# Kernel tuning notes

Measured on AMD Instinct MI355X. Metric: run time of the kernel, lower is better.

Reference implementation:

```python
import jax, jax.numpy as jnp
import numpy as np

MARGIN = 0.3
HARD_FACTOR = 0.0
NO_POS = 1000000.0
BIG = jnp.finfo(jnp.float32).max


def setup_inputs() -> dict:
    key = jax.random.key(0)
    k1, k2 = jax.random.split(key)
    global_feat = jax.random.normal(k1, (4096, 256), dtype=jnp.float32)
    labels = jax.random.randint(k2, (4096,), 0, 512, dtype=jnp.int64)
    return {"global_feat": global_feat, "labels": labels}


def euclidean_dist(x, y):
    # [m, n] pairwise distances via GEMM trick, clamped before sqrt
    xx = jnp.sum(x * x, axis=1, keepdims=True)          # [m, 1]
    yy = jnp.sum(y * y, axis=1, keepdims=True).T        # [1, n]
    d2 = xx + yy - 2.0 * (x @ y.T)
    return jnp.sqrt(jnp.maximum(d2, 1e-12))


def reference(global_feat, labels):
    feat = global_feat.astype(jnp.float32)
    dist_mat = euclidean_dist(feat, feat)               # [N, N]

    is_pos = labels[None, :] == labels[:, None]         # [N, N]
    is_neg = ~is_pos

    # hardest positive: masked row max; hardest negative: masked row min
    pos_max = jnp.max(jnp.where(is_pos, dist_mat, -BIG), axis=1)
    neg_min = jnp.min(jnp.where(is_neg, dist_mat, BIG), axis=1)
    has_pos = jnp.any(is_pos, axis=1)
    has_neg = jnp.any(is_neg, axis=1)
    dist_ap = jnp.where(has_pos, pos_max, NO_POS)
    dist_an = jnp.where(has_neg, neg_min, 0.0)

    dist_ap = dist_ap * (1.0 + HARD_FACTOR)
    dist_an = dist_an * (1.0 - HARD_FACTOR)

    valid = (dist_ap < NO_POS) & (dist_an > 0)
    n_valid = jnp.sum(valid.astype(jnp.float32))

    # MarginRankingLoss(y=1): mean over valid of relu(margin + dist_ap - dist_an)
    per_elem = jnp.maximum(MARGIN + dist_ap - dist_an, 0.0)
    loss_sum = jnp.sum(jnp.where(valid, per_elem, 0.0))
    loss = jnp.where(n_valid > 0, loss_sum / jnp.maximum(n_valid, 1.0), 0.0)
    return loss
```

## Files before the change

kernel.cpp:

```cpp
#include <hip/hip_runtime.h>
#include <hip/hip_bf16.h>

#define N 4096
#define D 256
#define MARGIN 0.3f
#define NSLOT 33
#define FLT_BIG 3.402823466e+38f

typedef __attribute__((ext_vector_type(8))) short short8;
typedef __attribute__((ext_vector_type(4))) float f32x4;
typedef const __attribute__((address_space(1))) unsigned char g1_t;
typedef __attribute__((address_space(3))) unsigned char l3_t;

__device__ __forceinline__ ushort f2bf(float f) {
    unsigned u = __float_as_uint(f);
    unsigned r = (u + 0x7fffu + ((u >> 16) & 1u)) >> 16;
    return (ushort)r;
}

__global__ __launch_bounds__(256) void prep_kernel(
        const float* __restrict__ feat,
        float* __restrict__ xx,
        ushort* __restrict__ hi,
        float* __restrict__ gacc,
        unsigned* __restrict__ ticket) {
    if (blockIdx.x == 0 && threadIdx.x == 0) {
        gacc[0] = 0.0f; gacc[1] = 0.0f; *ticket = 0u;
    }
    int row  = blockIdx.x * 4 + (threadIdx.x >> 6);
    int lane = threadIdx.x & 63;
    float4 v = *(const float4*)(feat + row * D + lane * 4);
    *(ushort4*)(hi + row * D + lane * 4) =
        make_ushort4(f2bf(v.x), f2bf(v.y), f2bf(v.z), f2bf(v.w));
    float s = v.x * v.x + v.y * v.y + v.z * v.z + v.w * v.w;
    #pragma unroll
    for (int off = 32; off >= 1; off >>= 1) s += __shfl_xor(s, off);
    if (lane == 0) xx[row] = s;
}

__global__ __launch_bounds__(256, 2) void dist_mfma_kernel(
        const ushort* __restrict__ hi,
        const int* __restrict__ labels, const float* __restrict__ xx,
        float* __restrict__ pPart, float* __restrict__ nPart) {
    __shared__ __attribute__((aligned(16))) short sA[2][128 * 64];
    __shared__ __attribute__((aligned(16))) short sB[2][128 * 64];
    __shared__ float rp[4][64], rn[4][64], cp[4][64], cn[4][64];

    int t = blockIdx.x, bi = 0, rem = 32;
    while (t >= rem) { t -= rem; ++bi; --rem; }
    const int bj = bi + t;
    const int rowBase = bi * 128;
    const int colBase = bj * 128;

    const int tid  = threadIdx.x;
    const int lane = tid & 63;
    const int wid  = tid >> 6;
    const int wr   = (wid >> 1) * 64;
    const int wc   = (wid & 1) * 64;
    const int l15  = lane & 15;
    const int kq   = (lane >> 4) * 8;
    const int swz  = (lane & 7) << 3;

    f32x4 acc[4][4] = {};

    auto stage = [&](int b, int kt) {
        #pragma unroll
        for (int i = 0; i < 4; ++i) {
            int c   = i * 256 + tid;
            int row = c >> 3;
            int kc  = ((c ^ row) & 7) * 8;
            __builtin_amdgcn_global_load_lds(
                (g1_t*)(hi + (size_t)(rowBase + row) * D + kt + kc),
                (l3_t*)(&sA[b][c * 8]), 16, 0, 0);
            __builtin_amdgcn_global_load_lds(
                (g1_t*)(hi + (size_t)(colBase + row) * D + kt + kc),
                (l3_t*)(&sB[b][c * 8]), 16, 0, 0);
        }
    };

    stage(0, 0);
    __syncthreads();
    int cur = 0;
    for (int step = 0; step < 4; ++step) {
        if (step < 3) stage(cur ^ 1, (step + 1) * 64);
        #pragma unroll
        for (int h = 0; h < 2; ++h) {
            short8 af[4], bfv[4];
            #pragma unroll
            for (int m = 0; m < 4; ++m) {
                int idx = ((wr + m * 16 + l15) << 6) + h * 32 + kq;
                af[m] = *(const short8*)(&sA[cur][idx ^ swz]);
            }
            #pragma unroll
            for (int n = 0; n < 4; ++n) {
                int idx = ((wc + n * 16 + l15) << 6) + h * 32 + kq;
                bfv[n] = *(const short8*)(&sB[cur][idx ^ swz]);
            }
            #pragma unroll
            for (int m = 0; m < 4; ++m)
                #pragma unroll
                for (int n = 0; n < 4; ++n)
                    acc[m][n] = __builtin_amdgcn_mfma_f32_16x16x32_bf16(
                        af[m], bfv[n], acc[m][n], 0, 0, 0);
        }
        __syncthreads();
        cur ^= 1;
    }

    float xr[4][4]; int lrow[4][4];
    #pragma unroll
    for (int m = 0; m < 4; ++m)
        #pragma unroll
        for (int j = 0; j < 4; ++j) {
            int rg = rowBase + wr + m * 16 + (lane >> 4) * 4 + j;
            xr[m][j] = xx[rg]; lrow[m][j] = labels[rg];
        }
    float xc[4]; int lcol[4];
    #pragma unroll
    for (int n = 0; n < 4; ++n) {
        int cg = colBase + wc + n * 16 + l15;
        xc[n] = xx[cg]; lcol[n] = labels[cg];
    }

    float pm2[4][4], nm2[4][4];
    float cpm[4],   cnm[4];
    #pragma unroll
    for (int m = 0; m < 4; ++m)
        #pragma unroll
        for (int j = 0; j < 4; ++j) { pm2[m][j] = 0.0f; nm2[m][j] = FLT_BIG; }
    #pragma unroll
    for (int n = 0; n < 4; ++n) { cpm[n] = 0.0f; cnm[n] = FLT_BIG; }

    #pragma unroll
    for (int m = 0; m < 4; ++m)
        #pragma unroll
        for (int n = 0; n < 4; ++n)
            #pragma unroll
            for (int j = 0; j < 4; ++j) {
                float d2 = fmaxf(xr[m][j] + xc[n] - 2.0f * acc[m][n][j], 0.0f);
                bool pos = (lrow[m][j] == lcol[n]);
                if (pos) {
                    pm2[m][j] = fmaxf(pm2[m][j], d2);
                    cpm[n]    = fmaxf(cpm[n],    d2);
                } else {
                    nm2[m][j] = fminf(nm2[m][j], d2);
                    cnm[n]    = fminf(cnm[n],    d2);
                }
            }

    #pragma unroll
    for (int m = 0; m < 4; ++m)
        #pragma unroll
        for (int j = 0; j < 4; ++j) {
            #pragma unroll
            for (int off = 1; off <= 8; off <<= 1) {
                pm2[m][j] = fmaxf(pm2[m][j], __shfl_xor(pm2[m][j], off));
                nm2[m][j] = fminf(nm2[m][j], __shfl_xor(nm2[m][j], off));
            }
        }
    #pragma unroll
    for (int n = 0; n < 4; ++n) {
        #pragma unroll
        for (int off = 16; off <= 32; off <<= 1) {
            cpm[n] = fmaxf(cpm[n], __shfl_xor(cpm[n], off));
            cnm[n] = fminf(cnm[n], __shfl_xor(cnm[n], off));
        }
    }

    if (l15 == 0) {
        #pragma unroll
        for (int m = 0; m < 4; ++m)
            #pragma unroll
            for (int j = 0; j < 4; ++j) {
                int r = m * 16 + (lane >> 4) * 4 + j;
                rp[wid][r] = pm2[m][j]; rn[wid][r] = nm2[m][j];
            }
    }
    if (lane < 16) {
        #pragma unroll
        for (int n = 0; n < 4; ++n) {
            int c = n * 16 + l15;
            cp[wid][c] = cpm[n]; cn[wid][c] = cnm[n];
        }
    }
    __syncthreads();

    if (tid < 128) {
        int half = tid >> 6, r = tid & 63;
        float p = fmaxf(rp[2 * half][r], rp[2 * half + 1][r]);
        float q = fminf(rn[2 * half][r], rn[2 * half + 1][r]);
        pPart[(size_t)(bj + 1) * N + rowBase + tid] = p;
        nPart[(size_t)(bj + 1) * N + rowBase + tid] = q;
    } else {
        int tc = tid - 128, half = tc >> 6, c = tc & 63;
        float p = fmaxf(cp[half][c], cp[half + 2][c]);
        float q = fminf(cn[half][c], cn[half + 2][c]);
        pPart[(size_t)bi * N + colBase + tc] = p;
        nPart[(size_t)bi * N + colBase + tc] = q;
    }
}

__global__ __launch_bounds__(256) void merge_kernel(
        const float* __restrict__ pPart, const float* __restrict__ nPart,
        float* __restrict__ gacc, unsigned* __restrict__ ticket,
        float* __restrict__ out) {
    __shared__ float ssum[4], scnt[4];
    int i = blockIdx.x * 256 + threadIdx.x;
    float ap2 = 0.0f, an2 = FLT_BIG;
    #pragma unroll 3
    for (int s = 0; s < NSLOT; ++s) {
        ap2 = fmaxf(ap2, pPart[(size_t)s * N + i]);
        an2 = fminf(an2, nPart[(size_t)s * N + i]);
    }
    float ap = sqrtf(fmaxf(ap2, 1e-12f));
    float an = sqrtf(fmaxf(an2, 1e-12f));
    bool valid = (ap < 1.0e6f) && (an > 0.0f);
    float per = valid ? fmaxf(MARGIN + ap - an, 0.0f) : 0.0f;
    float cnt = valid ? 1.0f : 0.0f;
    #pragma unroll
    for (int off = 32; off >= 1; off >>= 1) {
        per += __shfl_xor(per, off);
        cnt += __shfl_xor(cnt, off);
    }
    int tid = threadIdx.x, wv = tid >> 6;
    if ((tid & 63) == 0) { ssum[wv] = per; scnt[wv] = cnt; }
    __syncthreads();
    if (tid == 0) {
        float S = ssum[0] + ssum[1] + ssum[2] + ssum[3];
        float C = scnt[0] + scnt[1] + scnt[2] + scnt[3];
        atomicAdd(&gacc[0], S);
        atomicAdd(&gacc[1], C);
        __threadfence();
        unsigned tk = atomicAdd(ticket, 1u);
        if (tk == gridDim.x - 1) {
            float St = atomicAdd(&gacc[0], 0.0f);
            float Ct = atomicAdd(&gacc[1], 0.0f);
            out[0] = (Ct > 0.0f) ? St / fmaxf(Ct, 1.0f) : 0.0f;
        }
    }
}

extern "C" void kernel_launch(void* const* d_in, const int* in_sizes, int n_in,
                              void* d_out, int out_size, void* d_ws, size_t ws_size,
                              hipStream_t stream) {
    const float* feat = (const float*)d_in[0];
    const int* labels = (const int*)d_in[1];
    char* ws = (char*)d_ws;
    float*    xx     = (float*)ws;
    float*    gacc   = (float*)(ws + 16384);
    unsigned* ticket = (unsigned*)(ws + 16384 + 8);
    ushort*   hi     = (ushort*)(ws + 32768);
    float*    pPart  = (float*)(ws + 32768 + (size_t)N * D * 2);
    float*    nPart  = (float*)(ws + 32768 + (size_t)N * D * 2
                                + (size_t)NSLOT * N * 4);
    float* out = (float*)d_out;

    prep_kernel<<<N / 4, 256, 0, stream>>>(feat, xx, hi, gacc, ticket);
    dist_mfma_kernel<<<528, 256, 0, stream>>>(hi, labels, xx, pPart, nPart);
    merge_kernel<<<N / 256, 256, 0, stream>>>(pPart, nPart, gacc, ticket, out);
}
```

Measured before the change: 37.18 us.

## Shrink distance tiles to 64x64 and drop double buffering to raise occupancy

Halves the symmetric tile size from 128x128 to 64x64, which quadruples the block count from 528 to 2080. The double-buffered LDS staging is replaced by a single buffer with sync-load-compute, and launch bounds now ask for 6 blocks per CU. The intent is better load balance and more resident waves on the GPU. In exchange, each tile reuses less data and load latency is no longer overlapped. The partial-result slot count also roughly doubles, so the merge kernel reads 65 slots per row.

Result: faster. 36.00 us (-3.2%).

```diff
diff --git a/kernel.cpp b/kernel.cpp
--- a/kernel.cpp
+++ b/kernel.cpp
@@ -4,7 +4,8 @@
 #define N 4096
 #define D 256
 #define MARGIN 0.3f
-#define NSLOT 33
+#define NPANEL 64
+#define NSLOT 65
 #define FLT_BIG 3.402823466e+38f
 
 typedef __attribute__((ext_vector_type(8))) short short8;
@@ -38,103 +39,96 @@
     if (lane == 0) xx[row] = s;
 }
 
-__global__ __launch_bounds__(256, 2) void dist_mfma_kernel(
+__global__ __launch_bounds__(256, 6) void dist_mfma_kernel(
         const ushort* __restrict__ hi,
         const int* __restrict__ labels, const float* __restrict__ xx,
         float* __restrict__ pPart, float* __restrict__ nPart) {
-    __shared__ __attribute__((aligned(16))) short sA[2][128 * 64];
-    __shared__ __attribute__((aligned(16))) short sB[2][128 * 64];
-    __shared__ float rp[4][64], rn[4][64], cp[4][64], cn[4][64];
-
-    int t = blockIdx.x, bi = 0, rem = 32;
+    __shared__ __attribute__((aligned(16))) short sA[64 * 64];
+    __shared__ __attribute__((aligned(16))) short sB[64 * 64];
+    __shared__ float rp[4][32], rn[4][32], cp[4][32], cn[4][32];
+
+    int t = blockIdx.x, bi = 0, rem = NPANEL;
     while (t >= rem) { t -= rem; ++bi; --rem; }
     const int bj = bi + t;
-    const int rowBase = bi * 128;
-    const int colBase = bj * 128;
+    const int rowBase = bi * 64;
+    const int colBase = bj * 64;
 
     const int tid  = threadIdx.x;
     const int lane = tid & 63;
     const int wid  = tid >> 6;
-    const int wr   = (wid >> 1) * 64;
-    const int wc   = (wid & 1) * 64;
+    const int wr   = (wid >> 1) * 32;
+    const int wc   = (wid & 1) * 32;
     const int l15  = lane & 15;
     const int kq   = (lane >> 4) * 8;
     const int swz  = (lane & 7) << 3;
 
-    f32x4 acc[4][4] = {};
-
-    auto stage = [&](int b, int kt) {
-        #pragma unroll
-        for (int i = 0; i < 4; ++i) {
+    f32x4 acc[2][2] = {};
+
+    for (int kt = 0; kt < D; kt += 64) {
+        #pragma unroll
+        for (int i = 0; i < 2; ++i) {
             int c   = i * 256 + tid;
             int row = c >> 3;
             int kc  = ((c ^ row) & 7) * 8;
             __builtin_amdgcn_global_load_lds(
                 (g1_t*)(hi + (size_t)(rowBase + row) * D + kt + kc),
-                (l3_t*)(&sA[b][c * 8]), 16, 0, 0);
+                (l3_t*)(sA + c * 8), 16, 0, 0);
             __builtin_amdgcn_global_load_lds(
                 (g1_t*)(hi + (size_t)(colBase + row) * D + kt + kc),
-                (l3_t*)(&sB[b][c * 8]), 16, 0, 0);
-        }
-    };
-
-    stage(0, 0);
-    __syncthreads();
-    int cur = 0;
-    for (int step = 0; step < 4; ++step) {
-        if (step < 3) stage(cur ^ 1, (step + 1) * 64);
+                (l3_t*)(sB + c * 8), 16, 0, 0);
+        }
+        __syncthreads();
         #pragma unroll
         for (int h = 0; h < 2; ++h) {
-            short8 af[4], bfv[4];
-            #pragma unroll
-            for (int m = 0; m < 4; ++m) {
+            short8 af[2], bfv[2];
+            #pragma unroll
+            for (int m = 0; m < 2; ++m) {
                 int idx = ((wr + m * 16 + l15) << 6) + h * 32 + kq;
-                af[m] = *(const short8*)(&sA[cur][idx ^ swz]);
-            }
-            #pragma unroll
-            for (int n = 0; n < 4; ++n) {
+                af[m] = *(const short8*)(sA + (idx ^ swz));
+            }
+            #pragma unroll
+            for (int n = 0; n < 2; ++n) {
                 int idx = ((wc + n * 16 + l15) << 6) + h * 32 + kq;
-                bfv[n] = *(const short8*)(&sB[cur][idx ^ swz]);
-            }
-            #pragma unroll
-            for (int m = 0; m < 4; ++m)
+                bfv[n] = *(const short8*)(sB + (idx ^ swz));
+            }
+            #pragma unroll
+            for (int m = 0; m < 2; ++m)
                 #pragma unroll
-                for (int n = 0; n < 4; ++n)
+                for (int n = 0; n < 2; ++n)
                     acc[m][n] = __builtin_amdgcn_mfma_f32_16x16x32_bf16(
                         af[m], bfv[n], acc[m][n], 0, 0, 0);
         }
         __syncthreads();
-        cur ^= 1;
-    }
-
-    float xr[4][4]; int lrow[4][4];
-    #pragma unroll
-    for (int m = 0; m < 4; ++m)
+    }
+
+    float xr[2][4]; int lrow[2][4];
+    #pragma unroll
+    for (int m = 0; m < 2; ++m)
         #pragma unroll
         for (int j = 0; j < 4; ++j) {
             int rg = rowBase + wr + m * 16 + (lane >> 4) * 4 + j;
             xr[m][j] = xx[rg]; lrow[m][j] = labels[rg];
         }
-    float xc[4]; int lcol[4];
-    #pragma unroll
-    for (int n = 0; n < 4; ++n) {
+    float xc[2]; int lcol[2];
+    #pragma unroll
+    for (int n = 0; n < 2; ++n) {
         int cg = colBase + wc + n * 16 + l15;
         xc[n] = xx[cg]; lcol[n] = labels[cg];
     }
 
-    float pm2[4][4], nm2[4][4];
-    float cpm[4],   cnm[4];
-    #pragma unroll
-    for (int m = 0; m < 4; ++m)
+    float pm2[2][4], nm2[2][4];
+    float cpm[2],    cnm[2];
+    #pragma unroll
+    for (int m = 0; m < 2; ++m)
         #pragma unroll
         for (int j = 0; j < 4; ++j) { pm2[m][j] = 0.0f; nm2[m][j] = FLT_BIG; }
     #pragma unroll
-    for (int n = 0; n < 4; ++n) { cpm[n] = 0.0f; cnm[n] = FLT_BIG; }
-
-    #pragma unroll
-    for (int m = 0; m < 4; ++m)
-        #pragma unroll
-        for (int n = 0; n < 4; ++n)
+    for (int n = 0; n < 2; ++n) { cpm[n] = 0.0f; cnm[n] = FLT_BIG; }
+
+    #pragma unroll
+    for (int m = 0; m < 2; ++m)
+        #pragma unroll
+        for (int n = 0; n < 2; ++n)
             #pragma unroll
             for (int j = 0; j < 4; ++j) {
                 float d2 = fmaxf(xr[m][j] + xc[n] - 2.0f * acc[m][n][j], 0.0f);
@@ -149,7 +143,7 @@
             }
 
     #pragma unroll
-    for (int m = 0; m < 4; ++m)
+    for (int m = 0; m < 2; ++m)
         #pragma unroll
         for (int j = 0; j < 4; ++j) {
             #pragma unroll
@@ -159,7 +153,7 @@
             }
         }
     #pragma unroll
-    for (int n = 0; n < 4; ++n) {
+    for (int n = 0; n < 2; ++n) {
         #pragma unroll
         for (int off = 16; off <= 32; off <<= 1) {
             cpm[n] = fmaxf(cpm[n], __shfl_xor(cpm[n], off));
@@ -169,7 +163,7 @@
 
     if (l15 == 0) {
         #pragma unroll
-        for (int m = 0; m < 4; ++m)
+        for (int m = 0; m < 2; ++m)
             #pragma unroll
             for (int j = 0; j < 4; ++j) {
                 int r = m * 16 + (lane >> 4) * 4 + j;
@@ -178,25 +172,25 @@
     }
     if (lane < 16) {
         #pragma unroll
-        for (int n = 0; n < 4; ++n) {
+        for (int n = 0; n < 2; ++n) {
             int c = n * 16 + l15;
             cp[wid][c] = cpm[n]; cn[wid][c] = cnm[n];
         }
     }
     __syncthreads();
 
-    if (tid < 128) {
-        int half = tid >> 6, r = tid & 63;
-        float p = fmaxf(rp[2 * half][r], rp[2 * half + 1][r]);
-        float q = fminf(rn[2 * half][r], rn[2 * half + 1][r]);
-        pPart[(size_t)(bj + 1) * N + rowBase + tid] = p;
-        nPart[(size_t)(bj + 1) * N + rowBase + tid] = q;
-    } else {
-        int tc = tid - 128, half = tc >> 6, c = tc & 63;
-        float p = fmaxf(cp[half][c], cp[half + 2][c]);
-        float q = fminf(cn[half][c], cn[half + 2][c]);
-        pPart[(size_t)bi * N + colBase + tc] = p;
-        nPart[(size_t)bi * N + colBase + tc] = q;
+    if (tid < 64) {
+        int r = tid, pair = (r >> 5) * 2, rr = r & 31;
+        float p = fmaxf(rp[pair][rr], rp[pair + 1][rr]);
+        float q = fminf(rn[pair][rr], rn[pair + 1][rr]);
+        pPart[(size_t)(bj + 1) * N + rowBase + r] = p;
+        nPart[(size_t)(bj + 1) * N + rowBase + r] = q;
+    } else if (tid < 128) {
+        int c = tid - 64, pair = c >> 5, cc = c & 31;
+        float p = fmaxf(cp[pair][cc], cp[pair + 2][cc]);
+        float q = fminf(cn[pair][cc], cn[pair + 2][cc]);
+        pPart[(size_t)bi * N + colBase + c] = p;
+        nPart[(size_t)bi * N + colBase + c] = q;
     }
 }
 
@@ -207,7 +201,7 @@
     __shared__ float ssum[4], scnt[4];
     int i = blockIdx.x * 256 + threadIdx.x;
     float ap2 = 0.0f, an2 = FLT_BIG;
-    #pragma unroll 3
+    #pragma unroll 5
     for (int s = 0; s < NSLOT; ++s) {
         ap2 = fmaxf(ap2, pPart[(size_t)s * N + i]);
         an2 = fminf(an2, nPart[(size_t)s * N + i]);
@@ -256,6 +250,7 @@
     float* out = (float*)d_out;
 
     prep_kernel<<<N / 4, 256, 0, stream>>>(feat, xx, hi, gacc, ticket);
-    dist_mfma_kernel<<<528, 256, 0, stream>>>(hi, labels, xx, pPart, nPart);
+    dist_mfma_kernel<<<NPANEL * (NPANEL + 1) / 2, 256, 0, stream>>>(
+        hi, labels, xx, pPart, nPart);
     merge_kernel<<<N / 256, 256, 0, stream>>>(pPart, nPart, gacc, ticket, out);
 }
```
